# Performance work log

Hardware: AMD Instinct MI355X
Metric: run time of the kernel (lower is better)

Reference implementation:

```python
import jax, jax.numpy as jnp
import numpy as np

L, S, N, E, H = 2048, 2048, 4, 1024, 16
D = E // H


def setup_inputs() -> dict:
    k0 = jax.random.key(0)
    ks = jax.random.split(k0, 11)
    std = 1.0 / np.sqrt(E)
    return {
        "query": jax.random.normal(ks[0], (L, N, E), jnp.float32),
        "key": jax.random.normal(ks[1], (S, N, E), jnp.float32),
        "value": jax.random.normal(ks[2], (S, N, E), jnp.float32),
        "Wq": jax.random.normal(ks[3], (E, E), jnp.float32) * std,
        "bq": jnp.zeros((E,), jnp.float32),
        "Wk": jax.random.normal(ks[4], (E, E), jnp.float32) * std,
        "bk": jnp.zeros((E,), jnp.float32),
        "Wv": jax.random.normal(ks[5], (E, E), jnp.float32) * std,
        "bv": jnp.zeros((E,), jnp.float32),
        "Wo": jax.random.normal(ks[6], (E, E), jnp.float32) * std,
        "bo": jnp.zeros((E,), jnp.float32),
    }


def reference(query, key, value, Wq, bq, Wk, bk, Wv, bv, Wo, bo):
    # projections (torch Linear: x @ W.T + b)
    q = query @ Wq.T + bq  # [L,N,E]
    k = key @ Wk.T + bk    # [S,N,E]
    v = value @ Wv.T + bv  # [S,N,E]
    # split heads -> [N,H,len,D]
    q = q.reshape(L, N, H, D).transpose(1, 2, 0, 3)
    k = k.reshape(S, N, H, D).transpose(1, 2, 0, 3)
    v = v.reshape(S, N, H, D).transpose(1, 2, 0, 3)
    scores = jnp.einsum("nhld,nhsd->nhls", q, k) / np.sqrt(D).astype(np.float32)
    attn_weights = jax.nn.softmax(scores, axis=-1)  # [N,H,L,S]
    out = jnp.einsum("nhls,nhsd->nhld", attn_weights, v)  # [N,H,L,D]
    out = out.transpose(2, 0, 1, 3).reshape(L, N, E)
    attn_output = out @ Wo.T + bo  # [L,N,E]
    # need_weights=True, average_attn_weights=True -> mean over heads
    return attn_output, attn_weights.mean(axis=1)
```

## Files before the change

kernel.cpp:

```cpp
#include <hip/hip_runtime.h>
#include <hip/hip_bf16.h>

typedef __attribute__((ext_vector_type(8))) short short8;
typedef __attribute__((ext_vector_type(4))) float f32x4;

#define AS1 __attribute__((address_space(1)))
#define AS3 __attribute__((address_space(3)))

__device__ __forceinline__ void gload16(const void* g, void* l) {
  __builtin_amdgcn_global_load_lds((const AS1 unsigned int*)g,
                                   (AS3 unsigned int*)l, 16, 0, 0);
}

__device__ __forceinline__ unsigned short f2bf(float x) {
  unsigned u = __float_as_uint(x);
  u = (u + 0x7FFFu + ((u >> 16) & 1u)) >> 16;
  return (unsigned short)u;
}

__device__ __forceinline__ short8 lds8(const unsigned short* p) {
  return *(const short8*)p;
}

__device__ __forceinline__ short8 lds8s(const unsigned short* base, int row, int byteInRow) {
  const int a = (row << 7) + (byteInRow ^ ((row & 7) << 4));
  return *(const short8*)((const char*)base + a);
}

#define LL 2048
#define NB 4
#define EE 1024
#define HH 16
#define DD 64
#define MROWS 8192
#define SC2 0.18033688f

__global__ __launch_bounds__(256) void conv_bf16(const float* __restrict__ src,
                                                 unsigned short* __restrict__ dst) {
  int i = blockIdx.x * 256 + threadIdx.x;
  float4 v = ((const float4*)src)[i];
  ushort4 o;
  o.x = f2bf(v.x); o.y = f2bf(v.y); o.z = f2bf(v.z); o.w = f2bf(v.w);
  ((ushort4*)dst)[i] = o;
}

template <int MODE>
__global__ __launch_bounds__(256) void gemm_bt(const unsigned short* __restrict__ A,
                                               const unsigned short* __restrict__ B,
                                               const float* __restrict__ bias,
                                               unsigned short* __restrict__ outb,
                                               float* __restrict__ outf) {
  constexpr int K = 1024;
  __shared__ __align__(16) unsigned short As[128 * 32];
  __shared__ __align__(16) unsigned short Bs[128 * 32];
  const int tid = threadIdx.x;
  const int lane = tid & 63, w = tid >> 6;
  const int wr = w >> 1, wc = w & 1;
  const int lrow = lane & 15, lg = lane >> 4;
  const int m0 = blockIdx.y * 128, n0 = blockIdx.x * 128;

  f32x4 acc[4][4] = {};

  const int srow = tid >> 2, sseg = tid & 3;
  for (int k0 = 0; k0 < K; k0 += 32) {
    __syncthreads();
    const unsigned short* ga = A + (size_t)(m0 + srow) * K + k0 + sseg * 8;
    gload16(ga,            (char*)As + tid * 16);
    gload16(ga + 64 * K,   (char*)As + tid * 16 + 4096);
    const unsigned short* gb = B + (size_t)(n0 + srow) * K + k0 + sseg * 8;
    gload16(gb,            (char*)Bs + tid * 16);
    gload16(gb + 64 * K,   (char*)Bs + tid * 16 + 4096);
    __syncthreads();

    short8 af[4], bf[4];
#pragma unroll
    for (int mt = 0; mt < 4; ++mt)
      af[mt] = lds8(As + (wr * 64 + mt * 16 + lrow) * 32 + lg * 8);
#pragma unroll
    for (int nt = 0; nt < 4; ++nt)
      bf[nt] = lds8(Bs + (wc * 64 + nt * 16 + lrow) * 32 + lg * 8);
#pragma unroll
    for (int mt = 0; mt < 4; ++mt)
#pragma unroll
      for (int nt = 0; nt < 4; ++nt)
        acc[mt][nt] = __builtin_amdgcn_mfma_f32_16x16x32_bf16(af[mt], bf[nt],
                                                              acc[mt][nt], 0, 0, 0);
  }

#pragma unroll
  for (int mt = 0; mt < 4; ++mt) {
#pragma unroll
    for (int nt = 0; nt < 4; ++nt) {
      const int col = n0 + wc * 64 + nt * 16 + lrow;
      const float bv = bias[col];
#pragma unroll
      for (int r = 0; r < 4; ++r) {
        const int row = m0 + wr * 64 + mt * 16 + lg * 4 + r;
        const float v = acc[mt][nt][r] + bv;
        if (MODE == 0) {
          const int l = row >> 2, n = row & 3, h = col >> 6, d = col & 63;
          outb[(((size_t)(n * HH + h)) * LL + l) * DD + d] = f2bf(v);
        } else if (MODE == 1) {
          const int s = row >> 2, n = row & 3, h = col >> 6, d = col & 63;
          outb[(((size_t)(n * HH + h)) * DD + d) * LL + s] = f2bf(v);
        } else {
          outf[(size_t)row * EE + col] = v;
        }
      }
    }
  }
}

__global__ __launch_bounds__(256) void flash_attn(const unsigned short* __restrict__ qh,
                                                  const unsigned short* __restrict__ kh,
                                                  const unsigned short* __restrict__ vth,
                                                  unsigned short* __restrict__ oh,
                                                  float* __restrict__ mbuf,
                                                  float* __restrict__ zbuf) {
  __shared__ __align__(16) unsigned short Ks[2][64 * 64];
  __shared__ __align__(16) unsigned short Vts[2][64 * 64];
  __shared__ __align__(16) unsigned short QPs[64 * 64];
  const int tid = threadIdx.x, lane = tid & 63, w = tid >> 6;
  const int lrow = lane & 15, lg = lane >> 4;
  const int nh = blockIdx.y;
  const int l0 = blockIdx.x * 64;

  const unsigned short* qbase = qh + ((size_t)nh * LL + l0) * DD;
  const unsigned short* kbase = kh + (size_t)nh * LL * DD;
  const unsigned short* vbase = vth + (size_t)nh * DD * LL;

  const int sr = tid >> 3;
  const int cs = ((tid & 7) ^ (sr & 7)) * 8;

  gload16(qbase + (size_t)sr * DD + cs,        (char*)QPs + tid * 16);
  gload16(qbase + (size_t)(sr + 32) * DD + cs, (char*)QPs + tid * 16 + 4096);
  gload16(kbase + (size_t)sr * DD + cs,        (char*)Ks[0] + tid * 16);
  gload16(kbase + (size_t)(sr + 32) * DD + cs, (char*)Ks[0] + tid * 16 + 4096);
  gload16(vbase + (size_t)sr * LL + cs,        (char*)Vts[0] + tid * 16);
  gload16(vbase + (size_t)(sr + 32) * LL + cs, (char*)Vts[0] + tid * 16 + 4096);
  __syncthreads();

  short8 qa0 = lds8s(QPs, w * 16 + lrow, lg * 16);
  short8 qa1 = lds8s(QPs, w * 16 + lrow, 64 + lg * 16);

  float mrow = -1e30f, zrow = 0.f;
  f32x4 acco[4] = {};

  const int prow = w * 16 + lrow;
  int cur = 0;
  for (int s0 = 0; s0 < LL; s0 += 64) {
    if (s0 + 64 < LL) {
      const int nxt = cur ^ 1;
      const unsigned short* kt = kbase + (size_t)(s0 + 64) * DD;
      gload16(kt + (size_t)sr * DD + cs,        (char*)Ks[nxt] + tid * 16);
      gload16(kt + (size_t)(sr + 32) * DD + cs, (char*)Ks[nxt] + tid * 16 + 4096);
      gload16(vbase + (size_t)sr * LL + (s0 + 64) + cs,        (char*)Vts[nxt] + tid * 16);
      gload16(vbase + (size_t)(sr + 32) * LL + (s0 + 64) + cs, (char*)Vts[nxt] + tid * 16 + 4096);
    }

    f32x4 sc[4];
    __builtin_amdgcn_s_setprio(1);
#pragma unroll
    for (int ct = 0; ct < 4; ++ct) {
      short8 b0 = lds8s(Ks[cur], ct * 16 + lrow, lg * 16);
      short8 b1 = lds8s(Ks[cur], ct * 16 + lrow, 64 + lg * 16);
      f32x4 a = {};
      a = __builtin_amdgcn_mfma_f32_16x16x32_bf16(b0, qa0, a, 0, 0, 0);
      a = __builtin_amdgcn_mfma_f32_16x16x32_bf16(b1, qa1, a, 0, 0, 0);
      sc[ct] = a;
    }
    __builtin_amdgcn_s_setprio(0);

    float t = sc[0][0];
#pragma unroll
    for (int ct = 0; ct < 4; ++ct)
#pragma unroll
      for (int r = 0; r < 4; ++r) t = fmaxf(t, sc[ct][r]);
    t = fmaxf(t, __shfl_xor(t, 16));
    t = fmaxf(t, __shfl_xor(t, 32));
    const float tm = t * SC2;

    if (__any(tm > mrow + 8.0f)) {
      const float mnew = fmaxf(mrow, tm);
      const float f = __builtin_exp2f(mrow - mnew);
      mrow = mnew;
      zrow *= f;
#pragma unroll
      for (int dt = 0; dt < 4; ++dt)
#pragma unroll
        for (int r = 0; r < 4; ++r) acco[dt][r] *= f;
    }

    float ps = 0.f;
    unsigned int pk[8];
#pragma unroll
    for (int ct = 0; ct < 4; ++ct) {
      float e[4];
#pragma unroll
      for (int r = 0; r < 4; ++r) {
        e[r] = __builtin_exp2f(__builtin_fmaf(sc[ct][r], SC2, -mrow));
        ps += e[r];
      }
      pk[ct * 2 + 0] = (unsigned int)f2bf(e[0]) | ((unsigned int)f2bf(e[1]) << 16);
      pk[ct * 2 + 1] = (unsigned int)f2bf(e[2]) | ((unsigned int)f2bf(e[3]) << 16);
    }
    ps += __shfl_xor(ps, 16);
    ps += __shfl_xor(ps, 32);
    zrow += ps;

#pragma unroll
    for (int ct = 0; ct < 4; ++ct) {
      const int a = (prow << 7) + ((((ct * 2 + (lg >> 1)) ^ (prow & 7)) << 4) | ((lg & 1) << 3));
      uint2 u; u.x = pk[ct * 2]; u.y = pk[ct * 2 + 1];
      *(uint2*)((char*)QPs + a) = u;
    }

    short8 pa0 = lds8s(QPs, prow, lg * 16);
    short8 pa1 = lds8s(QPs, prow, 64 + lg * 16);
    __builtin_amdgcn_s_setprio(1);
#pragma unroll
    for (int dt = 0; dt < 4; ++dt) {
      short8 vb0 = lds8s(Vts[cur], dt * 16 + lrow, lg * 16);
      short8 vb1 = lds8s(Vts[cur], dt * 16 + lrow, 64 + lg * 16);
      acco[dt] = __builtin_amdgcn_mfma_f32_16x16x32_bf16(vb0, pa0, acco[dt], 0, 0, 0);
      acco[dt] = __builtin_amdgcn_mfma_f32_16x16x32_bf16(vb1, pa1, acco[dt], 0, 0, 0);
    }
    __builtin_amdgcn_s_setprio(0);
    __syncthreads();
    cur ^= 1;
  }

  const int n = nh >> 4, h = nh & 15;
  const int lt = l0 + w * 16 + lrow;
  const float rz = 1.0f / zrow;
#pragma unroll
  for (int dt = 0; dt < 4; ++dt) {
    ushort4 o;
    o.x = f2bf(acco[dt][0] * rz);
    o.y = f2bf(acco[dt][1] * rz);
    o.z = f2bf(acco[dt][2] * rz);
    o.w = f2bf(acco[dt][3] * rz);
    *(ushort4*)&oh[((size_t)lt * NB + n) * EE + h * 64 + dt * 16 + lg * 4] = o;
  }
  if (lg == 0) {
    mbuf[(size_t)nh * LL + lt] = mrow;
    zbuf[(size_t)nh * LL + lt] = zrow;
  }
}

__global__ __launch_bounds__(256) void mz_prep(const float* __restrict__ mbuf,
                                               const float* __restrict__ zbuf,
                                               float* __restrict__ cT) {
  const int i = blockIdx.x * 256 + threadIdx.x;
  const int nh = i >> 11, lt = i & 2047;
  const int n = nh >> 4, h = nh & 15;
  const float c = -(mbuf[i] + __builtin_log2f(zbuf[i]));
  cT[((size_t)n * LL + lt) * HH + h] = c;
}

__global__ __launch_bounds__(256) void weights_mean(const unsigned short* __restrict__ qh,
                                                    const unsigned short* __restrict__ kh,
                                                    const float* __restrict__ cT,
                                                    float* __restrict__ out1) {
  __shared__ __align__(16) unsigned short Qs[64 * 64];
  __shared__ __align__(16) unsigned short Ks[64 * 64];
  const int tid = threadIdx.x, lane = tid & 63, w = tid >> 6;
  const int lrow = lane & 15, lg = lane >> 4;
  const int n = blockIdx.z;
  const int l0 = blockIdx.y * 64, s0 = blockIdx.x * 64;

  const int sr = tid >> 3;
  const int cs = ((tid & 7) ^ (sr & 7)) * 8;

  float accw[4][4] = {};
  for (int h = 0; h < HH; ++h) {
    const int nh = n * HH + h;
    __syncthreads();
    const unsigned short* qbase = qh + ((size_t)nh * LL + l0) * DD;
    const unsigned short* kbase = kh + ((size_t)nh * LL + s0) * DD;
    gload16(qbase + (size_t)sr * DD + cs,        (char*)Qs + tid * 16);
    gload16(qbase + (size_t)(sr + 32) * DD + cs, (char*)Qs + tid * 16 + 4096);
    gload16(kbase + (size_t)sr * DD + cs,        (char*)Ks + tid * 16);
    gload16(kbase + (size_t)(sr + 32) * DD + cs, (char*)Ks + tid * 16 + 4096);
    __syncthreads();

    short8 qa0 = lds8s(Qs, w * 16 + lrow, lg * 16);
    short8 qa1 = lds8s(Qs, w * 16 + lrow, 64 + lg * 16);
    f32x4 sc[4];
    __builtin_amdgcn_s_setprio(1);
#pragma unroll
    for (int ct = 0; ct < 4; ++ct) {
      short8 b0 = lds8s(Ks, ct * 16 + lrow, lg * 16);
      short8 b1 = lds8s(Ks, ct * 16 + lrow, 64 + lg * 16);
      f32x4 a = {};
      a = __builtin_amdgcn_mfma_f32_16x16x32_bf16(qa0, b0, a, 0, 0, 0);
      a = __builtin_amdgcn_mfma_f32_16x16x32_bf16(qa1, b1, a, 0, 0, 0);
      sc[ct] = a;
    }
    __builtin_amdgcn_s_setprio(0);
#pragma unroll
    for (int r = 0; r < 4; ++r) {
      const int lt = l0 + w * 16 + lg * 4 + r;
      const float c = cT[((size_t)n * LL + lt) * HH + h];
#pragma unroll
      for (int ct = 0; ct < 4; ++ct)
        accw[ct][r] += __builtin_exp2f(__builtin_fmaf(sc[ct][r], SC2, c));
    }
  }
#pragma unroll
  for (int ct = 0; ct < 4; ++ct)
#pragma unroll
    for (int r = 0; r < 4; ++r) {
      const int lt = l0 + w * 16 + lg * 4 + r;
      const int s = s0 + ct * 16 + lrow;
      out1[((size_t)n * LL + lt) * LL + s] = accw[ct][r] * 0.0625f;
    }
}

extern "C" void kernel_launch(void* const* d_in, const int* in_sizes, int n_in,
                              void* d_out, int out_size, void* d_ws, size_t ws_size,
                              hipStream_t stream) {
  const float* query = (const float*)d_in[0];
  const float* key   = (const float*)d_in[1];
  const float* value = (const float*)d_in[2];
  const float* Wq = (const float*)d_in[3];
  const float* bq = (const float*)d_in[4];
  const float* Wk = (const float*)d_in[5];
  const float* bk = (const float*)d_in[6];
  const float* Wv = (const float*)d_in[7];
  const float* bv = (const float*)d_in[8];
  const float* Wo = (const float*)d_in[9];
  const float* bo = (const float*)d_in[10];

  float* out0 = (float*)d_out;
  float* out1 = out0 + (size_t)LL * NB * EE;

  char* ws = (char*)d_ws;
  unsigned short* xbuf = (unsigned short*)(ws + 0);
  unsigned short* wqb  = (unsigned short*)(ws + 16777216);
  unsigned short* wkb  = (unsigned short*)(ws + 18874368);
  unsigned short* wvb  = (unsigned short*)(ws + 20971520);
  unsigned short* wob  = (unsigned short*)(ws + 23068672);
  unsigned short* qhb  = (unsigned short*)(ws + 25165824);
  unsigned short* khb  = (unsigned short*)(ws + 41943040);
  unsigned short* vthb = (unsigned short*)(ws + 58720256);
  float* mbuf = (float*)(ws + 75497472);
  float* zbuf = (float*)(ws + 76021760);
  float* cT   = (float*)(ws + 76546048);

  const int nTok = MROWS * EE;
  const int nW   = EE * EE;

  conv_bf16<<<nW / 1024, 256, 0, stream>>>(Wq, wqb);
  conv_bf16<<<nW / 1024, 256, 0, stream>>>(Wk, wkb);
  conv_bf16<<<nW / 1024, 256, 0, stream>>>(Wv, wvb);
  conv_bf16<<<nW / 1024, 256, 0, stream>>>(Wo, wob);

  dim3 ggrid(EE / 128, MROWS / 128);

  conv_bf16<<<nTok / 1024, 256, 0, stream>>>(query, xbuf);
  gemm_bt<0><<<ggrid, 256, 0, stream>>>(xbuf, wqb, bq, qhb, nullptr);
  conv_bf16<<<nTok / 1024, 256, 0, stream>>>(key, xbuf);
  gemm_bt<0><<<ggrid, 256, 0, stream>>>(xbuf, wkb, bk, khb, nullptr);
  conv_bf16<<<nTok / 1024, 256, 0, stream>>>(value, xbuf);
  gemm_bt<1><<<ggrid, 256, 0, stream>>>(xbuf, wvb, bv, vthb, nullptr);

  flash_attn<<<dim3(LL / 64, NB * HH), 256, 0, stream>>>(qhb, khb, vthb, xbuf, mbuf, zbuf);

  gemm_bt<2><<<ggrid, 256, 0, stream>>>(xbuf, wob, bo, nullptr, out0);

  mz_prep<<<(NB * HH * LL) / 256, 256, 0, stream>>>(mbuf, zbuf, cT);

  weights_mean<<<dim3(LL / 64, LL / 64, NB), 256, 0, stream>>>(qhb, khb, cT, out1);
}
```

Before: 434.0 us.

## Double-buffer projection GEMM LDS tiles and tighten attention inner loop

```diff
diff --git a/kernel.cpp b/kernel.cpp
--- a/kernel.cpp
+++ b/kernel.cpp
@@ -51,8 +51,8 @@
                                                unsigned short* __restrict__ outb,
                                                float* __restrict__ outf) {
   constexpr int K = 1024;
-  __shared__ __align__(16) unsigned short As[128 * 32];
-  __shared__ __align__(16) unsigned short Bs[128 * 32];
+  __shared__ __align__(16) unsigned short As[2][64 * 64];
+  __shared__ __align__(16) unsigned short Bs[2][64 * 64];
   const int tid = threadIdx.x;
   const int lane = tid & 63, w = tid >> 6;
   const int wr = w >> 1, wc = w & 1;
@@ -61,30 +61,46 @@
 
   f32x4 acc[4][4] = {};
 
-  const int srow = tid >> 2, sseg = tid & 3;
+  const int sr = tid >> 3, sseg = tid & 7;
+  const int slog = sseg ^ (sr & 7);
+  const int mA = sr + 64 * (slog >> 2);
+  const int kof = (slog & 3) * 8;
+  const unsigned short* ga  = A + (size_t)(m0 + mA) * K + kof;
+  const unsigned short* ga2 = A + (size_t)(m0 + mA + 32) * K + kof;
+  const unsigned short* gb  = B + (size_t)(n0 + mA) * K + kof;
+  const unsigned short* gb2 = B + (size_t)(n0 + mA + 32) * K + kof;
+
+  gload16(ga,  (char*)As[0] + tid * 16);
+  gload16(ga2, (char*)As[0] + tid * 16 + 4096);
+  gload16(gb,  (char*)Bs[0] + tid * 16);
+  gload16(gb2, (char*)Bs[0] + tid * 16 + 4096);
+  __syncthreads();
+
+  int cur = 0;
   for (int k0 = 0; k0 < K; k0 += 32) {
+    if (k0 + 32 < K) {
+      const int nxt = cur ^ 1;
+      gload16(ga  + k0 + 32, (char*)As[nxt] + tid * 16);
+      gload16(ga2 + k0 + 32, (char*)As[nxt] + tid * 16 + 4096);
+      gload16(gb  + k0 + 32, (char*)Bs[nxt] + tid * 16);
+      gload16(gb2 + k0 + 32, (char*)Bs[nxt] + tid * 16 + 4096);
+    }
+
+    short8 af[4], bfr[4];
+#pragma unroll
+    for (int mt = 0; mt < 4; ++mt)
+      af[mt] = lds8s(As[cur], mt * 16 + lrow, (wr * 4 + lg) * 16);
+#pragma unroll
+    for (int nt = 0; nt < 4; ++nt)
+      bfr[nt] = lds8s(Bs[cur], nt * 16 + lrow, (wc * 4 + lg) * 16);
+#pragma unroll
+    for (int mt = 0; mt < 4; ++mt)
+#pragma unroll
+      for (int nt = 0; nt < 4; ++nt)
+        acc[mt][nt] = __builtin_amdgcn_mfma_f32_16x16x32_bf16(af[mt], bfr[nt],
+                                                              acc[mt][nt], 0, 0, 0);
     __syncthreads();
-    const unsigned short* ga = A + (size_t)(m0 + srow) * K + k0 + sseg * 8;
-    gload16(ga,            (char*)As + tid * 16);
-    gload16(ga + 64 * K,   (char*)As + tid * 16 + 4096);
-    const unsigned short* gb = B + (size_t)(n0 + srow) * K + k0 + sseg * 8;
-    gload16(gb,            (char*)Bs + tid * 16);
-    gload16(gb + 64 * K,   (char*)Bs + tid * 16 + 4096);
-    __syncthreads();
-
-    short8 af[4], bf[4];
-#pragma unroll
-    for (int mt = 0; mt < 4; ++mt)
-      af[mt] = lds8(As + (wr * 64 + mt * 16 + lrow) * 32 + lg * 8);
-#pragma unroll
-    for (int nt = 0; nt < 4; ++nt)
-      bf[nt] = lds8(Bs + (wc * 64 + nt * 16 + lrow) * 32 + lg * 8);
-#pragma unroll
-    for (int mt = 0; mt < 4; ++mt)
-#pragma unroll
-      for (int nt = 0; nt < 4; ++nt)
-        acc[mt][nt] = __builtin_amdgcn_mfma_f32_16x16x32_bf16(af[mt], bf[nt],
-                                                              acc[mt][nt], 0, 0, 0);
+    cur ^= 1;
   }
 
 #pragma unroll
@@ -146,16 +162,20 @@
   float mrow = -1e30f, zrow = 0.f;
   f32x4 acco[4] = {};
 
+  const unsigned short* kpre = kbase + (size_t)(64 + sr) * DD + cs;
+  const unsigned short* vpre = vbase + (size_t)sr * LL + 64 + cs;
+
   const int prow = w * 16 + lrow;
   int cur = 0;
   for (int s0 = 0; s0 < LL; s0 += 64) {
     if (s0 + 64 < LL) {
       const int nxt = cur ^ 1;
-      const unsigned short* kt = kbase + (size_t)(s0 + 64) * DD;
-      gload16(kt + (size_t)sr * DD + cs,        (char*)Ks[nxt] + tid * 16);
-      gload16(kt + (size_t)(sr + 32) * DD + cs, (char*)Ks[nxt] + tid * 16 + 4096);
-      gload16(vbase + (size_t)sr * LL + (s0 + 64) + cs,        (char*)Vts[nxt] + tid * 16);
-      gload16(vbase + (size_t)(sr + 32) * LL + (s0 + 64) + cs, (char*)Vts[nxt] + tid * 16 + 4096);
+      gload16(kpre,                       (char*)Ks[nxt] + tid * 16);
+      gload16(kpre + (size_t)32 * DD,     (char*)Ks[nxt] + tid * 16 + 4096);
+      gload16(vpre,                       (char*)Vts[nxt] + tid * 16);
+      gload16(vpre + (size_t)32 * LL,     (char*)Vts[nxt] + tid * 16 + 4096);
+      kpre += (size_t)64 * DD;
+      vpre += 64;
     }
 
     f32x4 sc[4];
@@ -171,11 +191,11 @@
     }
     __builtin_amdgcn_s_setprio(0);
 
-    float t = sc[0][0];
-#pragma unroll
-    for (int ct = 0; ct < 4; ++ct)
-#pragma unroll
-      for (int r = 0; r < 4; ++r) t = fmaxf(t, sc[ct][r]);
+    float q0 = fmaxf(fmaxf(fmaxf(sc[0][0], sc[0][1]), sc[0][2]), sc[0][3]);
+    float q1 = fmaxf(fmaxf(fmaxf(sc[1][0], sc[1][1]), sc[1][2]), sc[1][3]);
+    float q2 = fmaxf(fmaxf(fmaxf(sc[2][0], sc[2][1]), sc[2][2]), sc[2][3]);
+    float q3 = fmaxf(fmaxf(fmaxf(sc[3][0], sc[3][1]), sc[3][2]), sc[3][3]);
+    float t = fmaxf(fmaxf(fmaxf(q0, q1), q2), q3);
     t = fmaxf(t, __shfl_xor(t, 16));
     t = fmaxf(t, __shfl_xor(t, 32));
     const float tm = t * SC2;
@@ -201,8 +221,8 @@
         e[r] = __builtin_exp2f(__builtin_fmaf(sc[ct][r], SC2, -mrow));
         ps += e[r];
       }
-      pk[ct * 2 + 0] = (unsigned int)f2bf(e[0]) | ((unsigned int)f2bf(e[1]) << 16);
-      pk[ct * 2 + 1] = (unsigned int)f2bf(e[2]) | ((unsigned int)f2bf(e[3]) << 16);
+      asm("v_cvt_pk_bf16_f32 %0, %1, %2" : "=v"(pk[ct * 2 + 0]) : "v"(e[0]), "v"(e[1]));
+      asm("v_cvt_pk_bf16_f32 %0, %1, %2" : "=v"(pk[ct * 2 + 1]) : "v"(e[2]), "v"(e[3]));
     }
     ps += __shfl_xor(ps, 16);
     ps += __shfl_xor(ps, 32);
```

Result: faster. 411.8 us (-5.1%).
